# Kernel tuning notes

Measured on AMD Instinct MI355X. Metric: run time of the kernel, lower is better.

## Reference

```python
import jax, jax.numpy as jnp
import numpy as np

B, T, D, H, A, BIAS_DIM, E = 8, 1024, 1024, 16, 64, 32, 262144  # A = attention_dim_per_head


def setup_inputs() -> dict:
    key = jax.random.key(0)
    ks = jax.random.split(key, 10)
    states = jax.random.normal(ks[0], (B, T, D), dtype=jnp.float32)
    key_states = jax.random.normal(ks[1], (B, T, D), dtype=jnp.float32)
    masks = (jax.random.uniform(ks[2], (B, T, T)) < 0.1).astype(jnp.float32)
    # sparse bias edges: columns (edge_type, batch, query_idx, key_idx)
    et = jax.random.randint(ks[3], (E, 1), 0, BIAS_DIM)
    bi = jax.random.randint(ks[4], (E, 1), 0, B)
    qi = jax.random.randint(ks[5], (E, 1), 0, T)
    ki = jax.random.randint(ks[6], (E, 1), 0, T)
    attention_bias = jnp.concatenate([et, bi, qi, ki], axis=1).astype(jnp.int64)
    # parameters (xavier-like scale)
    def xav(k, shape, fan_in, fan_out):
        a = np.sqrt(6.0 / (fan_in + fan_out))
        return jax.random.uniform(k, shape, minval=-a, maxval=a, dtype=jnp.float32)
    Wq = xav(ks[7], (D, H, A), D, H * A)
    Wk = xav(jax.random.fold_in(ks[7], 1), (D, H, A), D, H * A)
    Wv = xav(jax.random.fold_in(ks[7], 2), (D, H, A), D, H * A)
    Wout = xav(ks[8], (H, A, D), H * A, D)
    bias_embs = xav(ks[9], (BIAS_DIM, A), BIAS_DIM, A)
    bias_scalar = xav(jax.random.fold_in(ks[9], 1), (A, 1), A, 1)
    return {"states": states, "key_states": key_states, "masks": masks,
            "attention_bias": attention_bias, "Wq": Wq, "Wk": Wk, "Wv": Wv,
            "Wout": Wout, "bias_embs": bias_embs, "bias_scalar": bias_scalar}


def reference(states, key_states, masks, attention_bias, Wq, Wk, Wv, Wout, bias_embs, bias_scalar):
    q = jnp.einsum('btd,dha->btha', states, Wq)
    k = jnp.einsum('btd,dha->btha', key_states, Wk)
    v = jnp.einsum('btd,dha->btha', key_states, Wv)
    alpha = jnp.einsum('bkha,bqha->bhqk', k, q)  # [B,H,Q,K]
    # sparse edge bias: embed edge types, project to scalar, scatter into [B,Q,K]
    bvals = (bias_embs[attention_bias[:, 0]] @ bias_scalar)[:, 0]  # [E]
    Bq, Hh, Q, K = alpha.shape
    bs = jnp.zeros((Bq, Q, K), dtype=alpha.dtype).at[
        attention_bias[:, 1], attention_bias[:, 2], attention_bias[:, 3]].set(bvals)
    ksum = k.sum(-1)  # [B,K,H]
    alpha = alpha + jnp.einsum('bqk,bkh->bhqk', bs, ksum)
    alpha = alpha * (1.0 / jnp.sqrt(jnp.float32(A)))
    alpha = alpha - masks[:, None, :, :] * jnp.finfo(jnp.float32).max
    alpha = jax.nn.softmax(alpha, axis=-1)
    context = jnp.einsum('bhqk,bkha->bqha', alpha, v)
    return jnp.einsum('btha,had->btd', context, Wout)
```

## Files before the change

### kernel.cpp

```cpp
#include <hip/hip_runtime.h>
#include <hip/hip_bf16.h>

#define BB 8
#define TT 1024
#define DD 1024
#define HH 16
#define AA 64
#define EE 262144

typedef unsigned short u16;
typedef unsigned int u32;
typedef short bf16x4 __attribute__((ext_vector_type(4)));
typedef short bf16x8 __attribute__((ext_vector_type(8)));
typedef float f32x4 __attribute__((ext_vector_type(4)));

__device__ __forceinline__ float bf2f(u16 u) {
    union { float f; u32 i; } c; c.i = ((u32)u) << 16; return c.f;
}
__device__ __forceinline__ u16 f2bf(float f) {
    union { float f; u32 i; } c; c.f = f;
    u32 x = c.i;
    return (u16)((x + 0x7FFFu + ((x >> 16) & 1u)) >> 16);
}
__device__ __forceinline__ u32 pack2bf(float a, float b) {
    union { __hip_bfloat162 h; u32 u; } c;
    c.h = __float22bfloat162_rn(float2{a, b});
    return c.u;
}

#define GLDS16(gp, lp)                                                        \
    __builtin_amdgcn_global_load_lds(                                         \
        (const __attribute__((address_space(1))) u32*)(const void*)(gp),      \
        (__attribute__((address_space(3))) u32*)(void*)(lp), 16, 0, 0)

#define MFMA(a, b, c) __builtin_amdgcn_mfma_f32_16x16x32_bf16((a), (b), (c), 0, 0, 0)

__global__ __launch_bounds__(256) void prep1(const float* __restrict__ states,
                                             const float* __restrict__ keys,
                                             const float* __restrict__ masks,
                                             const float* __restrict__ Wq,
                                             const float* __restrict__ Wk,
                                             const float* __restrict__ Wv,
                                             const float* __restrict__ Wout,
                                             u16* __restrict__ sbf,
                                             u16* __restrict__ kbf,
                                             u16* __restrict__ mb,
                                             int* __restrict__ idx,
                                             u16* __restrict__ wT) {
    __shared__ u16 t[64 * 72];
    int bi = blockIdx.x, tid = threadIdx.x;
    if (bi < 12288) {
        if (bi < 8192) {
            const float* src = (bi < 4096) ? states : keys;
            u16* dst = (bi < 4096) ? sbf : kbf;
            size_t i = ((size_t)(bi & 4095) * 256 + tid) * 8;
            f32x4 a = *(const f32x4*)(src + i);
            f32x4 b = *(const f32x4*)(src + i + 4);
            u32 o[4];
            o[0] = pack2bf(a[0], a[1]);
            o[1] = pack2bf(a[2], a[3]);
            o[2] = pack2bf(b[0], b[1]);
            o[3] = pack2bf(b[2], b[3]);
            *(bf16x8*)(dst + i) = *(bf16x8*)o;
        } else {
            size_t i = ((size_t)(bi - 8192) * 256 + tid) * 8;
            f32x4 a = *(const f32x4*)(masks + i);
            f32x4 b = *(const f32x4*)(masks + i + 4);
            const u16 M = f2bf(-1.0e30f);
            bf16x8 o;
#pragma unroll
            for (int j = 0; j < 4; j++) {
                o[j] = (short)((a[j] != 0.f) ? M : 0);
                o[4 + j] = (short)((b[j] != 0.f) ? M : 0);
            }
            *(bf16x8*)(mb + i) = o;
        }
    } else if (bi < 16384) {
        size_t i = ((size_t)(bi - 12288) * 256 + tid) * 8;
        int4 m1 = {-1, -1, -1, -1};
        *(int4*)(idx + i) = m1;
        *(int4*)(idx + i + 4) = m1;
    } else {
        int zb = bi - 16384;
        int z = zb >> 8, by = (zb >> 4) & 15, bx = zb & 15;
        const float* src = (z == 0) ? Wq : (z == 1) ? Wk : (z == 2) ? Wv : Wout;
        u16* dst = wT + (size_t)z * 1048576;
        int row0 = by * 64, col0 = bx * 64;
        int r = tid >> 2, c0 = (tid & 3) * 16;
        const float* sp = src + (size_t)(row0 + r) * 1024 + col0 + c0;
        f32x4 f0 = *(const f32x4*)(sp);
        f32x4 f1 = *(const f32x4*)(sp + 4);
        f32x4 f2_ = *(const f32x4*)(sp + 8);
        f32x4 f3 = *(const f32x4*)(sp + 12);
#pragma unroll
        for (int j = 0; j < 4; j++) {
            t[r * 72 + c0 + j] = f2bf(f0[j]);
            t[r * 72 + c0 + 4 + j] = f2bf(f1[j]);
            t[r * 72 + c0 + 8 + j] = f2bf(f2_[j]);
            t[r * 72 + c0 + 12 + j] = f2bf(f3[j]);
        }
        __syncthreads();
        bf16x8 o0, o1;
#pragma unroll
        for (int j = 0; j < 8; j++) o0[j] = (short)t[(c0 + j) * 72 + r];
#pragma unroll
        for (int j = 0; j < 8; j++) o1[j] = (short)t[(c0 + 8 + j) * 72 + r];
        *(bf16x8*)(dst + (size_t)(col0 + r) * 1024 + row0 + c0) = o0;
        *(bf16x8*)(dst + (size_t)(col0 + r) * 1024 + row0 + c0 + 8) = o1;
    }
}

__global__ __launch_bounds__(256) void scat_max(const int* __restrict__ ab,
                                                int* __restrict__ idx) {
    int e = blockIdx.x * 256 + threadIdx.x;
    int4 rec = ((const int4*)ab)[e];
    atomicMax(&idx[((((size_t)rec.y << 10) + rec.z) << 10) + rec.w], e);
}

__global__ __launch_bounds__(256) void scat_res(const int* __restrict__ ab,
                                                const int* __restrict__ idx,
                                                const float* __restrict__ be,
                                                const float* __restrict__ bsc,
                                                u16* __restrict__ mb) {
    __shared__ float proj[32];
    int tid = threadIdx.x;
    if (tid < 32) {
        float s = 0.f;
        for (int a = 0; a < 64; a++) s += be[tid * 64 + a] * bsc[a];
        proj[tid] = s * 0.125f;
    }
    __syncthreads();
    int e = blockIdx.x * 256 + tid;
    int4 rec = ((const int4*)ab)[e];
    size_t cell = ((((size_t)rec.y << 10) + rec.z) << 10) + rec.w;
    if (idx[cell] == e && bf2f(mb[cell]) > -1.0e29f) mb[cell] = f2bf(proj[rec.x]);
}

__global__ __launch_bounds__(256) void gemm5(const u16* __restrict__ sbf,
                                             const u16* __restrict__ kbf,
                                             const u16* __restrict__ wT,
                                             u16* __restrict__ qb,
                                             u16* __restrict__ kb,
                                             u16* __restrict__ vT,
                                             float* __restrict__ ks) {
    __shared__ u16 smem[17408];
    int tid = threadIdx.x;
    int wave = tid >> 6, lane = tid & 63;
    int quad = lane >> 4, l16 = lane & 15;
    int wm = wave >> 1, wn = wave & 1;
    int mat = blockIdx.x >> 3;
    int nloc = (blockIdx.x & 7) * 128;
    int mbase = blockIdx.y * 128;
    const u16* A = (mat == 0) ? sbf : kbf;
    const u16* BT = wT + (size_t)mat * 1048576;
    u16* Asm = smem;
    u16* Bsm = smem + 8192;
    f32x4 acc[4][4] = {};
    int srow = wave * 32 + (lane >> 3);
    int schunk = (lane & 7) ^ (lane >> 3);
    const u16* gA = A + (size_t)(mbase + srow) * 1024 + schunk * 8;
    const u16* gB = BT + (size_t)(nloc + srow) * 1024 + schunk * 8;
    u16* lA = Asm + wave * 2048;
    u16* lB = Bsm + wave * 2048;
    int sx = l16 & 7;
    for (int k0 = 0; k0 < 1024; k0 += 64) {
        __syncthreads();
#pragma unroll
        for (int j = 0; j < 4; j++) GLDS16(gA + k0 + j * 8192, lA + j * 512);
#pragma unroll
        for (int j = 0; j < 4; j++) GLDS16(gB + k0 + j * 8192, lB + j * 512);
        __syncthreads();
#pragma unroll
        for (int kk = 0; kk < 2; kk++) {
            bf16x8 af[4], bfr[4];
#pragma unroll
            for (int mt = 0; mt < 4; mt++)
                af[mt] = *(const bf16x8*)&Asm[(wm * 64 + mt * 16 + l16) * 64 +
                                              ((kk * 4 + quad) ^ sx) * 8];
#pragma unroll
            for (int nt = 0; nt < 4; nt++)
                bfr[nt] = *(const bf16x8*)&Bsm[(wn * 64 + nt * 16 + l16) * 64 +
                                               ((kk * 4 + quad) ^ sx) * 8];
#pragma unroll
            for (int mt = 0; mt < 4; mt++)
#pragma unroll
                for (int nt = 0; nt < 4; nt++)
                    acc[mt][nt] = MFMA(af[mt], bfr[nt], acc[mt][nt]);
        }
    }

    if (mat == 2) {
        __syncthreads();
#pragma unroll
        for (int mt = 0; mt < 4; mt++)
#pragma unroll
            for (int nt = 0; nt < 4; nt++)
#pragma unroll
                for (int r = 0; r < 4; r++) {
                    int rowl = wm * 64 + mt * 16 + quad * 4 + r;
                    int coll = wn * 64 + nt * 16 + l16;
                    smem[coll * 136 + rowl] = f2bf(acc[mt][nt][r]);
                }
        __syncthreads();
        int b = mbase >> 10, t0 = mbase & 1023;
        int c = tid >> 1, hf = tid & 1;
        int h = (nloc >> 6) + (c >> 6);
        int a = c & 63;
        u16* dst = vT + ((((size_t)(b * 16 + h)) * 64 + a) << 10) + t0 + hf * 64;
        const u16* srcl = smem + c * 136 + hf * 64;
#pragma unroll
        for (int j = 0; j < 8; j++) *(bf16x8*)(dst + j * 8) = *(const bf16x8*)(srcl + j * 8);
    } else {
        u16* dst = (mat == 0) ? qb : kb;
        float sc = (mat == 0) ? 0.125f : 1.0f;
#pragma unroll
        for (int mt = 0; mt < 4; mt++)
#pragma unroll
            for (int nt = 0; nt < 4; nt++)
#pragma unroll
                for (int r = 0; r < 4; r++) {
                    int gm = mbase + wm * 64 + mt * 16 + quad * 4 + r;
                    int gnl = nloc + wn * 64 + nt * 16 + l16;
                    int b = gm >> 10, t = gm & 1023, h = gnl >> 6, a = gnl & 63;
                    dst[(((size_t)(b * 16 + h) * 1024) + t) * 64 + a] =
                        f2bf(acc[mt][nt][r] * sc);
                }
        if (mat == 1) {
            int h = (nloc + wn * 64) >> 6;
#pragma unroll
            for (int mt = 0; mt < 4; mt++)
#pragma unroll
                for (int r = 0; r < 4; r++) {
                    float s = acc[mt][0][r] + acc[mt][1][r] + acc[mt][2][r] + acc[mt][3][r];
                    s += __shfl_xor(s, 1);
                    s += __shfl_xor(s, 2);
                    s += __shfl_xor(s, 4);
                    s += __shfl_xor(s, 8);
                    if (l16 == 0) {
                        int gm = mbase + wm * 64 + mt * 16 + quad * 4 + r;
                        int b = gm >> 10, t = gm & 1023;
                        ks[(((size_t)(b * 16 + h)) << 10) + t] = s;
                    }
                }
        }
    }
}

__global__ __launch_bounds__(256) void attn4(const u16* __restrict__ qbuf,
                                             const u16* __restrict__ kbuf,
                                             const u16* __restrict__ vT,
                                             const float* __restrict__ ksum,
                                             const u16* __restrict__ mb,
                                             u16* __restrict__ ctx) {
    __shared__ u16 Ksm[64 * 64];
    __shared__ u16 Vsm[64 * 64];
    __shared__ u16 Psm[4 * 16 * 72];
    __shared__ float sksm[64];
    __shared__ float lsm[64];
    int tid = threadIdx.x;
    int wave = tid >> 6, lane = tid & 63;
    int quad = lane >> 4, l16 = lane & 15;
    int qb = blockIdx.x, h = blockIdx.y, b = blockIdx.z;
    int bh = b * 16 + h;
    const u16* qp = qbuf + (size_t)bh * 65536;
    const u16* kp = kbuf + (size_t)bh * 65536;
    const u16* vp = vT + (size_t)bh * 65536;
    const float* ksp = ksum + (size_t)bh * 1024;
    int q0 = qb * 64 + wave * 16;
    const u16* mbp = mb + ((size_t)b * 1024 + q0 + l16) * 1024;

    bf16x8 qf0 = *(const bf16x8*)(qp + (size_t)(q0 + l16) * 64 + quad * 8);
    bf16x8 qf1 = *(const bf16x8*)(qp + (size_t)(q0 + l16) * 64 + 32 + quad * 8);

    f32x4 oacc[4] = {};
    float lsum = 0.f;
    int r8 = lane >> 3;
    int sch = (lane & 7) ^ r8;
    u16* lK = Ksm + wave * 1024;
    u16* lV = Vsm + wave * 1024;
    const u16* gK0 = kp + (size_t)(wave * 16 + r8) * 64 + sch * 8;
    const u16* gV0 = vp + (size_t)(wave * 16 + r8) * 1024 + sch * 8;
    int sx = l16 & 7;
    u16* pw = &Psm[wave * 16 * 72];

    for (int kb = 0; kb < 1024; kb += 64) {
        bf16x4 mraw[4];
#pragma unroll
        for (int nt = 0; nt < 4; nt++)
            mraw[nt] = *(const bf16x4*)(mbp + kb + nt * 16 + quad * 4);
        __syncthreads();
        GLDS16(gK0 + (size_t)kb * 64, lK);
        GLDS16(gK0 + (size_t)(kb + 8) * 64, lK + 512);
        GLDS16(gV0 + kb, lV);
        GLDS16(gV0 + 8 * 1024 + kb, lV + 512);
        if (tid < 64) sksm[tid] = ksp[kb + tid];
        __syncthreads();

        f32x4 sacc[4];
#pragma unroll
        for (int nt = 0; nt < 4; nt++) sacc[nt] = f32x4{-20.f, -20.f, -20.f, -20.f};
#pragma unroll
        for (int nt = 0; nt < 4; nt++) {
            bf16x8 kf0 = *(const bf16x8*)&Ksm[(nt * 16 + l16) * 64 + (quad ^ sx) * 8];
            bf16x8 kf1 = *(const bf16x8*)&Ksm[(nt * 16 + l16) * 64 + ((4 + quad) ^ sx) * 8];
            sacc[nt] = MFMA(kf0, qf0, sacc[nt]);
            sacc[nt] = MFMA(kf1, qf1, sacc[nt]);
        }

#pragma unroll
        for (int nt = 0; nt < 4; nt++) {
            f32x4 k4 = *(const f32x4*)&sksm[nt * 16 + quad * 4];
            float p[4];
#pragma unroll
            for (int r = 0; r < 4; r++) {
                float f = bf2f((u16)mraw[nt][r]);
                float e = __expf(sacc[nt][r] + f * k4[r]);
                p[r] = (f > -1.0e29f) ? e : 0.f;
                lsum += p[r];
            }
            *(u32*)&pw[l16 * 72 + nt * 16 + quad * 4] = pack2bf(p[0], p[1]);
            *(u32*)&pw[l16 * 72 + nt * 16 + quad * 4 + 2] = pack2bf(p[2], p[3]);
        }

#pragma unroll
        for (int hs = 0; hs < 2; hs++) {
            bf16x8 pf = *(const bf16x8*)&pw[l16 * 72 + hs * 32 + quad * 8];
#pragma unroll
            for (int at = 0; at < 4; at++) {
                bf16x8 vf = *(const bf16x8*)&Vsm[(at * 16 + l16) * 64 +
                                                 ((hs * 4 + quad) ^ sx) * 8];
                oacc[at] = MFMA(pf, vf, oacc[at]);
            }
        }
    }

    lsum += __shfl_xor(lsum, 16);
    lsum += __shfl_xor(lsum, 32);
    if (lane < 16) lsm[wave * 16 + lane] = lsum;
    __syncthreads();

#pragma unroll
    for (int r = 0; r < 4; r++) {
        float linv = 1.0f / lsm[wave * 16 + quad * 4 + r];
        int q = q0 + quad * 4 + r;
#pragma unroll
        for (int at = 0; at < 4; at++) {
            ctx[(((size_t)b * 1024 + q) * 16 + h) * 64 + at * 16 + l16] =
                f2bf(oacc[at][r] * linv);
        }
    }
}

__global__ __launch_bounds__(256) void gemmo(const u16* __restrict__ A,
                                             const u16* __restrict__ BT,
                                             float* __restrict__ C) {
    __shared__ u16 Asm[128 * 64];
    __shared__ u16 Bsm[128 * 64];
    int tid = threadIdx.x;
    int wave = tid >> 6, lane = tid & 63;
    int quad = lane >> 4, l16 = lane & 15;
    int wm = wave >> 1, wn = wave & 1;
    int mbase = blockIdx.y * 128, nbase = blockIdx.x * 128;
    f32x4 acc[4][4] = {};
    int srow = wave * 32 + (lane >> 3);
    int schunk = (lane & 7) ^ (lane >> 3);
    const u16* gA = A + (size_t)(mbase + srow) * 1024 + schunk * 8;
    const u16* gB = BT + (size_t)(nbase + srow) * 1024 + schunk * 8;
    u16* lA = Asm + wave * 2048;
    u16* lB = Bsm + wave * 2048;
    int sx = l16 & 7;
    for (int k0 = 0; k0 < 1024; k0 += 64) {
        __syncthreads();
#pragma unroll
        for (int j = 0; j < 4; j++) GLDS16(gA + k0 + j * 8192, lA + j * 512);
#pragma unroll
        for (int j = 0; j < 4; j++) GLDS16(gB + k0 + j * 8192, lB + j * 512);
        __syncthreads();
#pragma unroll
        for (int kk = 0; kk < 2; kk++) {
            bf16x8 af[4], bfr[4];
#pragma unroll
            for (int mt = 0; mt < 4; mt++)
                af[mt] = *(const bf16x8*)&Asm[(wm * 64 + mt * 16 + l16) * 64 +
                                              ((kk * 4 + quad) ^ sx) * 8];
#pragma unroll
            for (int nt = 0; nt < 4; nt++)
                bfr[nt] = *(const bf16x8*)&Bsm[(wn * 64 + nt * 16 + l16) * 64 +
                                               ((kk * 4 + quad) ^ sx) * 8];
#pragma unroll
            for (int mt = 0; mt < 4; mt++)
#pragma unroll
                for (int nt = 0; nt < 4; nt++)
                    acc[mt][nt] = MFMA(af[mt], bfr[nt], acc[mt][nt]);
        }
    }
#pragma unroll
    for (int mt = 0; mt < 4; mt++)
#pragma unroll
        for (int nt = 0; nt < 4; nt++)
#pragma unroll
            for (int r = 0; r < 4; r++) {
                int gm = mbase + wm * 64 + mt * 16 + quad * 4 + r;
                int gn = nbase + wn * 64 + nt * 16 + l16;
                C[(size_t)gm * 1024 + gn] = acc[mt][nt][r];
            }
}

extern "C" void kernel_launch(void* const* d_in, const int* in_sizes, int n_in,
                              void* d_out, int out_size, void* d_ws, size_t ws_size,
                              hipStream_t stream) {
    const float* states = (const float*)d_in[0];
    const float* key_states = (const float*)d_in[1];
    const float* masks = (const float*)d_in[2];
    const int* abias = (const int*)d_in[3];
    const float* Wq = (const float*)d_in[4];
    const float* Wk = (const float*)d_in[5];
    const float* Wv = (const float*)d_in[6];
    const float* Wout = (const float*)d_in[7];
    const float* be = (const float*)d_in[8];
    const float* bsc = (const float*)d_in[9];

    char* ws = (char*)d_ws;
    size_t off = 0;
    auto alloc = [&](size_t n) { void* p = ws + off; off += (n + 255) & ~(size_t)255; return p; };
    u16* wT = (u16*)alloc(4ull * 1024 * 1024 * 2);
    u16* sbf = (u16*)alloc((size_t)BB * TT * DD * 2);
    u16* kbf = (u16*)alloc((size_t)BB * TT * DD * 2);
    u16* qb_ = (u16*)alloc((size_t)BB * HH * TT * AA * 2);
    u16* kb_ = (u16*)alloc((size_t)BB * HH * TT * AA * 2);
    u16* vT_ = (u16*)alloc((size_t)BB * HH * AA * TT * 2);
    float* ks_ = (float*)alloc((size_t)BB * HH * TT * 4);
    u16* mb_ = (u16*)alloc((size_t)BB * TT * TT * 2);

    u16* woT = wT + 3145728;
    int* idx_ = (int*)qb_;
    u16* ctx_ = sbf;

    prep1<<<dim3(17408), 256, 0, stream>>>(states, key_states, masks, Wq, Wk, Wv,
                                           Wout, sbf, kbf, mb_, idx_, wT);
    scat_max<<<dim3(EE / 256), 256, 0, stream>>>(abias, idx_);
    scat_res<<<dim3(EE / 256), 256, 0, stream>>>(abias, idx_, be, bsc, mb_);
    gemm5<<<dim3(24, 64), 256, 0, stream>>>(sbf, kbf, wT, qb_, kb_, vT_, ks_);
    attn4<<<dim3(16, 16, 8), 256, 0, stream>>>(qb_, kb_, vT_, ks_, mb_, ctx_);
    gemmo<<<dim3(8, 64), 256, 0, stream>>>(ctx_, woT, (float*)d_out);
}
```

Measured before the change: 369.9 us.

## Double-buffer K/V tiles in attention and switch softmax to exp2

The attention kernel now double-buffers its K and V tiles in LDS. It prefetches the next tile with global-to-LDS loads and fetches the next mask and key-sum values into registers while the current tile is computed. This replaces the two full block barriers per iteration with a raw barrier plus a partial vmcnt wait, so load latency is meant to overlap with the MFMA work. The Q scale and bias projection now fold in log2(e), so the kernel can use the hardware exp2 instruction. The fixed softmax offset is rescaled to match, and the key-sum shared buffer and the final __syncthreads are removed. The hand-counted vmcnt and the dropped barrier both depend on the exact order of loads and on memory being visible within a wave.

Result: slower. 386.8 us (+4.6%).

```diff
diff --git a/kernel.cpp b/kernel.cpp
--- a/kernel.cpp
+++ b/kernel.cpp
@@ -27,6 +27,18 @@
     c.h = __float22bfloat162_rn(float2{a, b});
     return c.u;
 }
+__device__ __forceinline__ float fast_exp2(float x) {
+#if __has_builtin(__builtin_amdgcn_exp2f)
+    return __builtin_amdgcn_exp2f(x);
+#else
+    float r;
+    asm("v_exp_f32 %0, %1" : "=v"(r) : "v"(x));
+    return r;
+#endif
+}
+
+#define QSCALE 0.18033688f
+#define SOFT_OFF -28.8539008f
 
 #define GLDS16(gp, lp)                                                        \
     __builtin_amdgcn_global_load_lds(                                         \
@@ -34,6 +46,8 @@
         (__attribute__((address_space(3))) u32*)(void*)(lp), 16, 0, 0)
 
 #define MFMA(a, b, c) __builtin_amdgcn_mfma_f32_16x16x32_bf16((a), (b), (c), 0, 0, 0)
+
+#define MEMFENCE asm volatile("" ::: "memory")
 
 __global__ __launch_bounds__(256) void prep1(const float* __restrict__ states,
                                              const float* __restrict__ keys,
@@ -127,7 +141,7 @@
     if (tid < 32) {
         float s = 0.f;
         for (int a = 0; a < 64; a++) s += be[tid * 64 + a] * bsc[a];
-        proj[tid] = s * 0.125f;
+        proj[tid] = s * QSCALE;
     }
     __syncthreads();
     int e = blockIdx.x * 256 + tid;
@@ -212,7 +226,7 @@
         for (int j = 0; j < 8; j++) *(bf16x8*)(dst + j * 8) = *(const bf16x8*)(srcl + j * 8);
     } else {
         u16* dst = (mat == 0) ? qb : kb;
-        float sc = (mat == 0) ? 0.125f : 1.0f;
+        float sc = (mat == 0) ? QSCALE : 1.0f;
 #pragma unroll
         for (int mt = 0; mt < 4; mt++)
 #pragma unroll
@@ -246,16 +260,15 @@
     }
 }
 
-__global__ __launch_bounds__(256) void attn4(const u16* __restrict__ qbuf,
+__global__ __launch_bounds__(256) void attn5(const u16* __restrict__ qbuf,
                                              const u16* __restrict__ kbuf,
                                              const u16* __restrict__ vT,
                                              const float* __restrict__ ksum,
                                              const u16* __restrict__ mb,
                                              u16* __restrict__ ctx) {
-    __shared__ u16 Ksm[64 * 64];
-    __shared__ u16 Vsm[64 * 64];
+    __shared__ u16 Ksm[2][64 * 64];
+    __shared__ u16 Vsm[2][64 * 64];
     __shared__ u16 Psm[4 * 16 * 72];
-    __shared__ float sksm[64];
     __shared__ float lsm[64];
     int tid = threadIdx.x;
     int wave = tid >> 6, lane = tid & 63;
@@ -276,45 +289,80 @@
     float lsum = 0.f;
     int r8 = lane >> 3;
     int sch = (lane & 7) ^ r8;
-    u16* lK = Ksm + wave * 1024;
-    u16* lV = Vsm + wave * 1024;
     const u16* gK0 = kp + (size_t)(wave * 16 + r8) * 64 + sch * 8;
     const u16* gV0 = vp + (size_t)(wave * 16 + r8) * 1024 + sch * 8;
     int sx = l16 & 7;
     u16* pw = &Psm[wave * 16 * 72];
 
-    for (int kb = 0; kb < 1024; kb += 64) {
-        bf16x4 mraw[4];
+    bf16x4 mraw[4];
+    f32x4 k4[4];
+#pragma unroll
+    for (int nt = 0; nt < 4; nt++)
+        mraw[nt] = *(const bf16x4*)(mbp + nt * 16 + quad * 4);
+#pragma unroll
+    for (int nt = 0; nt < 4; nt++)
+        k4[nt] = *(const f32x4*)(ksp + nt * 16 + quad * 4);
+    {
+        u16* lK = &Ksm[0][wave * 1024];
+        u16* lV = &Vsm[0][wave * 1024];
+        GLDS16(gK0, lK);
+        GLDS16(gK0 + 8 * 64, lK + 512);
+        GLDS16(gV0, lV);
+        GLDS16(gV0 + 8 * 1024, lV + 512);
+    }
+
+    for (int it = 0; it < 16; it++) {
+        int c = it & 1;
+        int kn = (it < 15) ? (it + 1) * 64 : it * 64;
+
+        bf16x4 mrawN[4];
+        f32x4 k4N[4];
 #pragma unroll
         for (int nt = 0; nt < 4; nt++)
-            mraw[nt] = *(const bf16x4*)(mbp + kb + nt * 16 + quad * 4);
-        __syncthreads();
-        GLDS16(gK0 + (size_t)kb * 64, lK);
-        GLDS16(gK0 + (size_t)(kb + 8) * 64, lK + 512);
-        GLDS16(gV0 + kb, lV);
-        GLDS16(gV0 + 8 * 1024 + kb, lV + 512);
-        if (tid < 64) sksm[tid] = ksp[kb + tid];
-        __syncthreads();
+            mrawN[nt] = *(const bf16x4*)(mbp + kn + nt * 16 + quad * 4);
+#pragma unroll
+        for (int nt = 0; nt < 4; nt++)
+            k4N[nt] = *(const f32x4*)(ksp + kn + nt * 16 + quad * 4);
+
+        MEMFENCE;
+        __builtin_amdgcn_s_barrier();
+        MEMFENCE;
+
+        {
+            u16* lK = &Ksm[c ^ 1][wave * 1024];
+            u16* lV = &Vsm[c ^ 1][wave * 1024];
+            GLDS16(gK0 + (size_t)kn * 64, lK);
+            GLDS16(gK0 + (size_t)(kn + 8) * 64, lK + 512);
+            GLDS16(gV0 + kn, lV);
+            GLDS16(gV0 + 8 * 1024 + kn, lV + 512);
+        }
+        asm volatile("s_waitcnt vmcnt(12)" ::: "memory");
+        __builtin_amdgcn_s_barrier();
+        MEMFENCE;
+
+        const u16* Kc = &Ksm[c][0];
+        const u16* Vc = &Vsm[c][0];
 
         f32x4 sacc[4];
 #pragma unroll
-        for (int nt = 0; nt < 4; nt++) sacc[nt] = f32x4{-20.f, -20.f, -20.f, -20.f};
+        for (int nt = 0; nt < 4; nt++)
+            sacc[nt] = f32x4{SOFT_OFF, SOFT_OFF, SOFT_OFF, SOFT_OFF};
 #pragma unroll
         for (int nt = 0; nt < 4; nt++) {
-            bf16x8 kf0 = *(const bf16x8*)&Ksm[(nt * 16 + l16) * 64 + (quad ^ sx) * 8];
-            bf16x8 kf1 = *(const bf16x8*)&Ksm[(nt * 16 + l16) * 64 + ((4 + quad) ^ sx) * 8];
+            bf16x8 kf0 = *(const bf16x8*)&Kc[(nt * 16 + l16) * 64 + (quad ^ sx) * 8];
+            bf16x8 kf1 = *(const bf16x8*)&Kc[(nt * 16 + l16) * 64 + ((4 + quad) ^ sx) * 8];
             sacc[nt] = MFMA(kf0, qf0, sacc[nt]);
             sacc[nt] = MFMA(kf1, qf1, sacc[nt]);
         }
 
 #pragma unroll
         for (int nt = 0; nt < 4; nt++) {
-            f32x4 k4 = *(const f32x4*)&sksm[nt * 16 + quad * 4];
             float p[4];
 #pragma unroll
             for (int r = 0; r < 4; r++) {
                 float f = bf2f((u16)mraw[nt][r]);
-                float e = __expf(sacc[nt][r] + f * k4[r]);
+                float x = fmaf(f, k4[nt][r], sacc[nt][r]);
+                float e = fast_exp2(x);
                 p[r] = (f > -1.0e29f) ? e : 0.f;
                 lsum += p[r];
             }
@@ -327,17 +375,22 @@
             bf16x8 pf = *(const bf16x8*)&pw[l16 * 72 + hs * 32 + quad * 8];
 #pragma unroll
             for (int at = 0; at < 4; at++) {
-                bf16x8 vf = *(const bf16x8*)&Vsm[(at * 16 + l16) * 64 +
-                                                 ((hs * 4 + quad) ^ sx) * 8];
+                bf16x8 vf = *(const bf16x8*)&Vc[(at * 16 + l16) * 64 +
+                                                ((hs * 4 + quad) ^ sx) * 8];
                 oacc[at] = MFMA(pf, vf, oacc[at]);
             }
+        }
+
+#pragma unroll
+        for (int nt = 0; nt < 4; nt++) {
+            mraw[nt] = mrawN[nt];
+            k4[nt] = k4N[nt];
         }
     }
 
     lsum += __shfl_xor(lsum, 16);
     lsum += __shfl_xor(lsum, 32);
     if (lane < 16) lsm[wave * 16 + lane] = lsum;
-    __syncthreads();
 
 #pragma unroll
     for (int r = 0; r < 4; r++) {
@@ -441,6 +494,6 @@
     scat_max<<<dim3(EE / 256), 256, 0, stream>>>(abias, idx_);
     scat_res<<<dim3(EE / 256), 256, 0, stream>>>(abias, idx_, be, bsc, mb_);
     gemm5<<<dim3(24, 64), 256, 0, stream>>>(sbf, kbf, wT, qb_, kb_, vT_, ks_);
-    attn4<<<dim3(16, 16, 8), 256, 0, stream>>>(qb_, kb_, vT_, ks_, mb_, ctx_);
+    attn5<<<dim3(16, 16, 8), 256, 0, stream>>>(qb_, kb_, vT_, ks_, mb_, ctx_);
     gemmo<<<dim3(8, 64), 256, 0, stream>>>(ctx_, woT, (float*)d_out);
 }
```

## Load K/V fragments directly from global and switch softmax to exp2

Applied to the files above, without the earlier changes.

The attention kernel no longer stages K and V tiles (and the key-sum vector) through shared memory. Each wave now reads its MFMA fragments straight from global memory, which removes both block-wide barriers per key block. The query scale and bias projection are folded with log2(e) so the softmax can use the hardware exp2 instruction, with a matching fixed offset. The cost is that the four waves of a block all fetch the same K/V data, so they rely on the L1/L2 caches. The direct V loads are strided row reads, and nothing prefetches ahead of the MFMAs.

Result: slower. 579.7 us (+56.7%).

```diff
diff --git a/kernel.cpp b/kernel.cpp
--- a/kernel.cpp
+++ b/kernel.cpp
@@ -27,6 +27,18 @@
     c.h = __float22bfloat162_rn(float2{a, b});
     return c.u;
 }
+__device__ __forceinline__ float fast_exp2(float x) {
+#if __has_builtin(__builtin_amdgcn_exp2f)
+    return __builtin_amdgcn_exp2f(x);
+#else
+    float r;
+    asm("v_exp_f32 %0, %1" : "=v"(r) : "v"(x));
+    return r;
+#endif
+}
+
+#define QSCALE 0.18033688f
+#define SOFT_OFF -28.8539008f
 
 #define GLDS16(gp, lp)                                                        \
     __builtin_amdgcn_global_load_lds(                                         \
@@ -127,7 +139,7 @@
     if (tid < 32) {
         float s = 0.f;
         for (int a = 0; a < 64; a++) s += be[tid * 64 + a] * bsc[a];
-        proj[tid] = s * 0.125f;
+        proj[tid] = s * QSCALE;
     }
     __syncthreads();
     int e = blockIdx.x * 256 + tid;
@@ -212,7 +224,7 @@
         for (int j = 0; j < 8; j++) *(bf16x8*)(dst + j * 8) = *(const bf16x8*)(srcl + j * 8);
     } else {
         u16* dst = (mat == 0) ? qb : kb;
-        float sc = (mat == 0) ? 0.125f : 1.0f;
+        float sc = (mat == 0) ? QSCALE : 1.0f;
 #pragma unroll
         for (int mt = 0; mt < 4; mt++)
 #pragma unroll
@@ -246,16 +258,13 @@
     }
 }
 
-__global__ __launch_bounds__(256) void attn4(const u16* __restrict__ qbuf,
+__global__ __launch_bounds__(256) void attn6(const u16* __restrict__ qbuf,
                                              const u16* __restrict__ kbuf,
                                              const u16* __restrict__ vT,
                                              const float* __restrict__ ksum,
                                              const u16* __restrict__ mb,
                                              u16* __restrict__ ctx) {
-    __shared__ u16 Ksm[64 * 64];
-    __shared__ u16 Vsm[64 * 64];
     __shared__ u16 Psm[4 * 16 * 72];
-    __shared__ float sksm[64];
     __shared__ float lsm[64];
     int tid = threadIdx.x;
     int wave = tid >> 6, lane = tid & 63;
@@ -274,47 +283,42 @@
 
     f32x4 oacc[4] = {};
     float lsum = 0.f;
-    int r8 = lane >> 3;
-    int sch = (lane & 7) ^ r8;
-    u16* lK = Ksm + wave * 1024;
-    u16* lV = Vsm + wave * 1024;
-    const u16* gK0 = kp + (size_t)(wave * 16 + r8) * 64 + sch * 8;
-    const u16* gV0 = vp + (size_t)(wave * 16 + r8) * 1024 + sch * 8;
-    int sx = l16 & 7;
     u16* pw = &Psm[wave * 16 * 72];
+
+    const u16* kfp = kp + (size_t)l16 * 64 + quad * 8;
+    const u16* vfp = vp + (size_t)l16 * 1024 + quad * 8;
 
     for (int kb = 0; kb < 1024; kb += 64) {
         bf16x4 mraw[4];
+        f32x4 k4[4];
 #pragma unroll
         for (int nt = 0; nt < 4; nt++)
             mraw[nt] = *(const bf16x4*)(mbp + kb + nt * 16 + quad * 4);
-        __syncthreads();
-        GLDS16(gK0 + (size_t)kb * 64, lK);
-        GLDS16(gK0 + (size_t)(kb + 8) * 64, lK + 512);
-        GLDS16(gV0 + kb, lV);
-        GLDS16(gV0 + 8 * 1024 + kb, lV + 512);
-        if (tid < 64) sksm[tid] = ksp[kb + tid];
-        __syncthreads();
+#pragma unroll
+        for (int nt = 0; nt < 4; nt++)
+            k4[nt] = *(const f32x4*)(ksp + kb + nt * 16 + quad * 4);
 
         f32x4 sacc[4];
 #pragma unroll
-        for (int nt = 0; nt < 4; nt++) sacc[nt] = f32x4{-20.f, -20.f, -20.f, -20.f};
+        for (int nt = 0; nt < 4; nt++)
+            sacc[nt] = f32x4{SOFT_OFF, SOFT_OFF, SOFT_OFF, SOFT_OFF};
 #pragma unroll
         for (int nt = 0; nt < 4; nt++) {
-            bf16x8 kf0 = *(const bf16x8*)&Ksm[(nt * 16 + l16) * 64 + (quad ^ sx) * 8];
-            bf16x8 kf1 = *(const bf16x8*)&Ksm[(nt * 16 + l16) * 64 + ((4 + quad) ^ sx) * 8];
+            const u16* kr = kfp + (size_t)(kb + nt * 16) * 64;
+            bf16x8 kf0 = *(const bf16x8*)(kr);
+            bf16x8 kf1 = *(const bf16x8*)(kr + 32);
             sacc[nt] = MFMA(kf0, qf0, sacc[nt]);
             sacc[nt] = MFMA(kf1, qf1, sacc[nt]);
         }
 
 #pragma unroll
         for (int nt = 0; nt < 4; nt++) {
-            f32x4 k4 = *(const f32x4*)&sksm[nt * 16 + quad * 4];
             float p[4];
 #pragma unroll
             for (int r = 0; r < 4; r++) {
                 float f = bf2f((u16)mraw[nt][r]);
-                float e = __expf(sacc[nt][r] + f * k4[r]);
+                float x = fmaf(f, k4[nt][r], sacc[nt][r]);
+                float e = fast_exp2(x);
                 p[r] = (f > -1.0e29f) ? e : 0.f;
                 lsum += p[r];
             }
@@ -327,8 +331,8 @@
             bf16x8 pf = *(const bf16x8*)&pw[l16 * 72 + hs * 32 + quad * 8];
 #pragma unroll
             for (int at = 0; at < 4; at++) {
-                bf16x8 vf = *(const bf16x8*)&Vsm[(at * 16 + l16) * 64 +
-                                                 ((hs * 4 + quad) ^ sx) * 8];
+                bf16x8 vf = *(const bf16x8*)(vfp + (size_t)(at * 16) * 1024 +
+                                             kb + hs * 32);
                 oacc[at] = MFMA(pf, vf, oacc[at]);
             }
         }
@@ -337,7 +341,6 @@
     lsum += __shfl_xor(lsum, 16);
     lsum += __shfl_xor(lsum, 32);
     if (lane < 16) lsm[wave * 16 + lane] = lsum;
-    __syncthreads();
 
 #pragma unroll
     for (int r = 0; r < 4; r++) {
@@ -441,6 +444,6 @@
     scat_max<<<dim3(EE / 256), 256, 0, stream>>>(abias, idx_);
     scat_res<<<dim3(EE / 256), 256, 0, stream>>>(abias, idx_, be, bsc, mb_);
     gemm5<<<dim3(24, 64), 256, 0, stream>>>(sbf, kbf, wT, qb_, kb_, vT_, ks_);
-    attn4<<<dim3(16, 16, 8), 256, 0, stream>>>(qb_, kb_, vT_, ks_, mb_, ctx_);
+    attn6<<<dim3(16, 16, 8), 256, 0, stream>>>(qb_, kb_, vT_, ks_, mb_, ctx_);
     gemmo<<<dim3(8, 64), 256, 0, stream>>>(ctx_, woT, (float*)d_out);
 }
```
